# Performance work log

Measured on AMD Instinct MI355X. Metric: run time of the kernel, lower is better.

Reference implementation:

```python
import jax, jax.numpy as jnp
import numpy as np

B, T, C, H = 2, 2048, 1024, 16
HD = C // H  # 64

def setup_inputs() -> dict:
    key = jax.random.key(0)
    ks = jax.random.split(key, 9)
    s = 0.02
    return {
        "x": jax.random.normal(ks[0], (B, T, C), jnp.float32),
        "Wq": jax.random.normal(ks[1], (C, C), jnp.float32) * s,
        "bq": jax.random.normal(ks[2], (C,), jnp.float32) * s,
        "Wk": jax.random.normal(ks[3], (C, C), jnp.float32) * s,
        "bk": jax.random.normal(ks[4], (C,), jnp.float32) * s,
        "Wv": jax.random.normal(ks[5], (C, C), jnp.float32) * s,
        "bv": jax.random.normal(ks[6], (C,), jnp.float32) * s,
        "Wp": jax.random.normal(ks[7], (C, C), jnp.float32) * s,
        "bp": jax.random.normal(ks[8], (C,), jnp.float32) * s,
    }

def reference(x, Wq, bq, Wk, bk, Wv, bv, Wp, bp):
    Bb, Tt, Cc = x.shape
    hd = Cc // H
    # project and split heads: [B, H, T, hd]
    def heads(W, b):
        return (x @ W.T + b).reshape(Bb, Tt, H, hd).transpose(0, 2, 1, 3)
    q, k, v = heads(Wq, bq), heads(Wk, bk), heads(Wv, bv)
    scale = 1.0 / np.sqrt(hd).astype(np.float32)
    att = jnp.einsum('bhqd,bhkd->bhqk', q, k) * scale
    causal = jnp.tril(jnp.ones((Tt, Tt), bool))
    att = jnp.where(causal[None, None], att, -jnp.inf)
    att = jax.nn.softmax(att, axis=-1)
    y = jnp.einsum('bhqk,bhkd->bhqd', att, v)
    y = y.transpose(0, 2, 1, 3).reshape(Bb, Tt, Cc)
    return y @ Wp.T + bp
```

## Files before the change

kernel.cpp:

```cpp
#include <hip/hip_runtime.h>
#include <hip/hip_bf16.h>

#define Tsz 2048
#define Csz 1024
#define Hn 16

typedef short s8v __attribute__((ext_vector_type(8)));
typedef short s4v __attribute__((ext_vector_type(4)));
typedef float f4v __attribute__((ext_vector_type(4)));
typedef int   i4v __attribute__((ext_vector_type(4)));
typedef unsigned u2v __attribute__((ext_vector_type(2)));

#define QSCALE (0.125f * 1.44269504088896f)

__device__ __forceinline__ unsigned short bfr(float x) {
    return (unsigned short)((__builtin_bit_cast(unsigned, x) + 0x8000u) >> 16);
}
__device__ __forceinline__ unsigned pack2_rn(float a, float b) {
    const unsigned ua = __builtin_bit_cast(unsigned, a) + 0x8000u;
    const unsigned ub = __builtin_bit_cast(unsigned, b) + 0x8000u;
    return (ua >> 16) | (ub & 0xFFFF0000u);
}

__device__ __forceinline__ void gload_lds(const void* g, void* l) {
    __builtin_amdgcn_global_load_lds(
        (const __attribute__((address_space(1))) void*)g,
        (__attribute__((address_space(3))) void*)l, 16, 0, 0);
}

__global__ void cvt6(const float* __restrict__ x, const float* __restrict__ wq,
                     const float* __restrict__ wk, const float* __restrict__ wv,
                     const float* __restrict__ wp,
                     short* __restrict__ xo, short* __restrict__ qo,
                     short* __restrict__ ko, short* __restrict__ vo,
                     short* __restrict__ po) {
    const int bx = blockIdx.x;
    const float* in; short* out; int ib;
    if (bx < 4096) { in = x; out = xo; ib = bx; }
    else {
        const int r = bx - 4096, w = r >> 10;
        ib = r & 1023;
        switch (w) {
            case 0: in = wq; out = qo; break;
            case 1: in = wk; out = ko; break;
            case 2: in = wv; out = vo; break;
            default: in = wp; out = po; break;
        }
    }
    const int i = ib * 1024 + threadIdx.x * 4;
    float4 v = *(const float4*)(in + i);
    int2 o;
    o.x = (int)pack2_rn(v.x, v.y);
    o.y = (int)pack2_rn(v.z, v.w);
    *(int2*)(out + i) = o;
}

__global__ __launch_bounds__(256, 3) void qkv_gemm(
    const short* __restrict__ X,
    const short* __restrict__ Wq, const short* __restrict__ Wk, const short* __restrict__ Wv,
    const float* __restrict__ bq, const float* __restrict__ bk, const float* __restrict__ bv,
    short* __restrict__ Qo, short* __restrict__ Ko, short* __restrict__ Vto)
{
    const int z = blockIdx.z;
    const short* W = (z == 0) ? Wq : (z == 1) ? Wk : Wv;
    const float* bias = (z == 0) ? bq : (z == 1) ? bk : bv;

    __shared__ __align__(16) short Ash[128 * 32];
    __shared__ __align__(16) short Bsh[128 * 32];
    __shared__ __align__(16) short TR[64 * 72];

    const int tid = threadIdx.x, lane = tid & 63, wave = tid >> 6;
    const int ln = lane & 15, hi = lane >> 4;
    const int m0 = blockIdx.x * 128, n0 = blockIdx.y * 128;
    const int wm = (wave >> 1) * 64, wn = (wave & 1) * 64;

    const short* Ag = X + (size_t)(m0 + (tid >> 2)) * Csz + (tid & 3) * 8;
    const short* Bg = W + (size_t)(n0 + (tid >> 2)) * Csz + (tid & 3) * 8;

    f4v acc[4][4];
    #pragma unroll
    for (int mt = 0; mt < 4; mt++)
        #pragma unroll
        for (int nt = 0; nt < 4; nt++)
            #pragma unroll
            for (int i = 0; i < 4; i++) acc[mt][nt][i] = 0.f;

    for (int k0 = 0; k0 < Csz; k0 += 32) {
        __syncthreads();
        gload_lds(Ag + k0, Ash + tid * 8);
        gload_lds(Ag + k0 + (size_t)64 * Csz, Ash + 2048 + tid * 8);
        gload_lds(Bg + k0, Bsh + tid * 8);
        gload_lds(Bg + k0 + (size_t)64 * Csz, Bsh + 2048 + tid * 8);
        __syncthreads();

        s8v af[4], bfr_[4];
        #pragma unroll
        for (int mt = 0; mt < 4; mt++)
            af[mt] = *(const s8v*)(Ash + (wm + mt * 16 + ln) * 32 + hi * 8);
        #pragma unroll
        for (int nt = 0; nt < 4; nt++)
            bfr_[nt] = *(const s8v*)(Bsh + (wn + nt * 16 + ln) * 32 + hi * 8);
        #pragma unroll
        for (int mt = 0; mt < 4; mt++)
            #pragma unroll
            for (int nt = 0; nt < 4; nt++)
                acc[mt][nt] = __builtin_amdgcn_mfma_f32_16x16x32_bf16(af[mt], bfr_[nt], acc[mt][nt], 0, 0, 0);
    }

    if (z == 2) {
        const int b = m0 >> 11, t0 = m0 & 2047;
        float bvv[4];
        #pragma unroll
        for (int nt = 0; nt < 4; nt++) bvv[nt] = bias[n0 + wn + nt * 16 + ln];
        #pragma unroll
        for (int ph = 0; ph < 4; ph++) {
            const int mh = ph >> 1, nh = ph & 1;
            __syncthreads();
            if ((wave >> 1) == mh && (wave & 1) == nh) {
                #pragma unroll
                for (int mt = 0; mt < 4; mt++)
                    #pragma unroll
                    for (int nt = 0; nt < 4; nt++) {
                        int2 pk;
                        pk.x = (int)pack2_rn(acc[mt][nt][0] + bvv[nt], acc[mt][nt][1] + bvv[nt]);
                        pk.y = (int)pack2_rn(acc[mt][nt][2] + bvv[nt], acc[mt][nt][3] + bvv[nt]);
                        *(int2*)(TR + (nt * 16 + ln) * 72 + mt * 16 + hi * 4) = pk;
                    }
            }
            __syncthreads();
            const int chl = tid >> 2, seg = tid & 3;
            const s8v r0 = *(const s8v*)(TR + chl * 72 + seg * 16);
            const s8v r1 = *(const s8v*)(TR + chl * 72 + seg * 16 + 8);
            short* dst = Vto + (size_t)(b * 1024 + n0 + nh * 64 + chl) * Tsz + t0 + mh * 64 + seg * 16;
            *(s8v*)(dst) = r0;
            *(s8v*)(dst + 8) = r1;
        }
        return;
    }

    const float scale = (z == 0) ? QSCALE : 1.0f;
    short* out = (z == 0) ? Qo : Ko;

    #pragma unroll
    for (int nt = 0; nt < 4; nt++) {
        const int col = n0 + wn + nt * 16 + ln;
        const float bvv = bias[col];
        #pragma unroll
        for (int mt = 0; mt < 4; mt++) {
            const int row0 = m0 + wm + mt * 16 + hi * 4;
            #pragma unroll
            for (int i = 0; i < 4; i++)
                out[(size_t)(row0 + i) * Csz + col] = (short)bfr((acc[mt][nt][i] + bvv) * scale);
        }
    }
}

__global__ __launch_bounds__(256, 2) void proj_gemm(
    const short* __restrict__ A, const short* __restrict__ W,
    const float* __restrict__ bias, float* __restrict__ out)
{
    __shared__ __align__(16) short Ash[128 * 32];
    __shared__ __align__(16) short Bsh[64 * 32];

    const int tid = threadIdx.x, lane = tid & 63, wave = tid >> 6;
    const int ln = lane & 15, hi = lane >> 4;
    const int m0 = blockIdx.x * 128, n0 = blockIdx.y * 64;
    const int wm = (wave >> 1) * 64, wn = (wave & 1) * 32;

    const short* Ag = A + (size_t)(m0 + (tid >> 2)) * Csz + (tid & 3) * 8;
    const short* Bg = W + (size_t)(n0 + (tid >> 2)) * Csz + (tid & 3) * 8;

    f4v acc[4][2];
    #pragma unroll
    for (int mt = 0; mt < 4; mt++)
        #pragma unroll
        for (int nt = 0; nt < 2; nt++)
            #pragma unroll
            for (int i = 0; i < 4; i++) acc[mt][nt][i] = 0.f;

    for (int k0 = 0; k0 < Csz; k0 += 32) {
        __syncthreads();
        gload_lds(Ag + k0, Ash + tid * 8);
        gload_lds(Ag + k0 + (size_t)64 * Csz, Ash + 2048 + tid * 8);
        gload_lds(Bg + k0, Bsh + tid * 8);
        __syncthreads();

        s8v af[4], bfr_[2];
        #pragma unroll
        for (int mt = 0; mt < 4; mt++)
            af[mt] = *(const s8v*)(Ash + (wm + mt * 16 + ln) * 32 + hi * 8);
        #pragma unroll
        for (int nt = 0; nt < 2; nt++)
            bfr_[nt] = *(const s8v*)(Bsh + (wn + nt * 16 + ln) * 32 + hi * 8);
        #pragma unroll
        for (int mt = 0; mt < 4; mt++)
            #pragma unroll
            for (int nt = 0; nt < 2; nt++)
                acc[mt][nt] = __builtin_amdgcn_mfma_f32_16x16x32_bf16(af[mt], bfr_[nt], acc[mt][nt], 0, 0, 0);
    }

    #pragma unroll
    for (int nt = 0; nt < 2; nt++) {
        const int col = n0 + wn + nt * 16 + ln;
        const float bvv = bias[col];
        #pragma unroll
        for (int mt = 0; mt < 4; mt++)
            #pragma unroll
            for (int i = 0; i < 4; i++)
                out[(size_t)(m0 + wm + mt * 16 + hi * 4 + i) * Csz + col] = acc[mt][nt][i] + bvv;
    }
}

__global__ __launch_bounds__(256, 4) void attn14(
    const short* __restrict__ Q, const short* __restrict__ Kg,
    const short* __restrict__ Vt, short* __restrict__ Y)
{
    __shared__ __align__(16) short Ksh[64 * 64];
    __shared__ __align__(16) short Vsh[64 * 64];

    const int tid = threadIdx.x, lane = tid & 63, wave = tid >> 6;
    const int ln = lane & 15, hi = lane >> 4;

    const int n = blockIdx.x;
    const int c = n & 255, j = n >> 8;
    const int bh = (j << 3) | (c >> 5);
    const int t = c & 31;
    const int qt = (j & 1) ? t : 31 - t;

    const size_t base = (size_t)(bh >> 4) * Tsz * Csz + (size_t)(bh & 15) * 64;
    const size_t vtbase = (size_t)bh * 64 * Tsz;
    const int qrel = wave * 16 + ln;

    s8v qf[2];
    #pragma unroll
    for (int kk = 0; kk < 2; kk++)
        qf[kk] = *(const s8v*)(Q + base + (size_t)(qt * 64 + qrel) * Csz + kk * 32 + hi * 8);

    f4v o[4];
    float lsum = 0.f;
    #pragma unroll
    for (int dt = 0; dt < 4; dt++)
        #pragma unroll
        for (int i = 0; i < 4; i++) o[dt][i] = 0.f;

    const int sr = tid >> 3, scs = tid & 7;
    const short* Kp = Kg + base + (size_t)sr * Csz + scs * 8;
    const short* Vp = Vt + vtbase + (size_t)sr * Tsz + scs * 8;
    const int swo = sr * 64 + (scs ^ (sr & 7)) * 8;
    const int nkb = qt + 1;

    int foff[2][4];
    #pragma unroll
    for (int nt = 0; nt < 4; nt++)
        #pragma unroll
        for (int kk = 0; kk < 2; kk++)
            foff[kk][nt] = (nt * 16 + ln) * 64 + (((kk * 4 + hi) ^ (ln & 7)) * 8);

    s8v k0 = *(const s8v*)(Kp);
    s8v k1 = *(const s8v*)(Kp + (size_t)32 * Csz);
    s8v v0 = *(const s8v*)(Vp);
    s8v v1 = *(const s8v*)(Vp + (size_t)32 * Tsz);
    *(s8v*)(&Ksh[swo]) = k0;
    *(s8v*)(&Ksh[swo + 32 * 64]) = k1;
    *(s8v*)(&Vsh[swo]) = v0;
    *(s8v*)(&Vsh[swo + 32 * 64]) = v1;
    __syncthreads();

    for (int kb = 0; kb < nkb; kb++) {
        const bool more = (kb + 1 < nkb);
        if (more) {
            const size_t ko = (size_t)(kb + 1) * 64;
            k0 = *(const s8v*)(Kp + ko * Csz);
            k1 = *(const s8v*)(Kp + (ko + 32) * Csz);
            v0 = *(const s8v*)(Vp + ko);
            v1 = *(const s8v*)(Vp + ko + (size_t)32 * Tsz);
        }

        s8v kf[2][4], vf[2][4];
        #pragma unroll
        for (int nt = 0; nt < 4; nt++)
            #pragma unroll
            for (int kk = 0; kk < 2; kk++) {
                kf[kk][nt] = *(const s8v*)(&Ksh[foff[kk][nt]]);
                vf[kk][nt] = *(const s8v*)(&Vsh[foff[kk][nt]]);
            }

        f4v s[4];
        #pragma unroll
        for (int nt = 0; nt < 4; nt++) {
            #pragma unroll
            for (int i = 0; i < 4; i++) s[nt][i] = 0.f;
            s[nt] = __builtin_amdgcn_mfma_f32_16x16x32_bf16(kf[0][nt], qf[0], s[nt], 0, 0, 0);
            s[nt] = __builtin_amdgcn_mfma_f32_16x16x32_bf16(kf[1][nt], qf[1], s[nt], 0, 0, 0);
        }

        const bool dg = !more;
        unsigned pw[4][2];
        #pragma unroll
        for (int nt = 0; nt < 4; nt++) {
            float pv[4];
            #pragma unroll
            for (int i = 0; i < 4; i++) pv[i] = exp2f(s[nt][i]);
            if (dg) {
                const int kr = nt * 16 + hi * 4;
                #pragma unroll
                for (int i = 0; i < 4; i++)
                    if (kr + i > qrel) pv[i] = 0.f;
            }
            lsum += (pv[0] + pv[1]) + (pv[2] + pv[3]);
            pw[nt][0] = pack2_rn(pv[0], pv[1]);
            pw[nt][1] = pack2_rn(pv[2], pv[3]);
        }

        u2v r0a = __builtin_amdgcn_permlane32_swap(pw[0][0], pw[1][0], false, false);
        u2v r0b = __builtin_amdgcn_permlane16_swap(r0a[0], r0a[1], false, false);
        u2v r1a = __builtin_amdgcn_permlane32_swap(pw[0][1], pw[1][1], false, false);
        u2v r1b = __builtin_amdgcn_permlane16_swap(r1a[0], r1a[1], false, false);
        u2v r2a = __builtin_amdgcn_permlane32_swap(pw[2][0], pw[3][0], false, false);
        u2v r2b = __builtin_amdgcn_permlane16_swap(r2a[0], r2a[1], false, false);
        u2v r3a = __builtin_amdgcn_permlane32_swap(pw[2][1], pw[3][1], false, false);
        u2v r3b = __builtin_amdgcn_permlane16_swap(r3a[0], r3a[1], false, false);
        i4v p0 = { (int)r0b[0], (int)r1b[0], (int)r0b[1], (int)r1b[1] };
        i4v p1 = { (int)r2b[0], (int)r3b[0], (int)r2b[1], (int)r3b[1] };
        const s8v pb0 = __builtin_bit_cast(s8v, p0);
        const s8v pb1 = __builtin_bit_cast(s8v, p1);

        #pragma unroll
        for (int dt = 0; dt < 4; dt++) {
            o[dt] = __builtin_amdgcn_mfma_f32_16x16x32_bf16(vf[0][dt], pb0, o[dt], 0, 0, 0);
            o[dt] = __builtin_amdgcn_mfma_f32_16x16x32_bf16(vf[1][dt], pb1, o[dt], 0, 0, 0);
        }

        if (more) {
            __syncthreads();
            *(s8v*)(&Ksh[swo]) = k0;
            *(s8v*)(&Ksh[swo + 32 * 64]) = k1;
            *(s8v*)(&Vsh[swo]) = v0;
            *(s8v*)(&Vsh[swo + 32 * 64]) = v1;
            __syncthreads();
        }
    }

    float l = lsum;
    l += __shfl_xor(l, 16);
    l += __shfl_xor(l, 32);
    const float inv = 1.0f / l;
    const int qrow = qt * 64 + qrel;
    #pragma unroll
    for (int dt = 0; dt < 4; dt++) {
        int2 w;
        w.x = (int)pack2_rn(o[dt][0] * inv, o[dt][1] * inv);
        w.y = (int)pack2_rn(o[dt][2] * inv, o[dt][3] * inv);
        *(int2*)(Y + base + (size_t)qrow * Csz + dt * 16 + hi * 4) = w;
    }
}

extern "C" void kernel_launch(void* const* d_in, const int* in_sizes, int n_in,
                              void* d_out, int out_size, void* d_ws, size_t ws_size,
                              hipStream_t stream) {
    const float* x  = (const float*)d_in[0];
    const float* Wq = (const float*)d_in[1];
    const float* bq = (const float*)d_in[2];
    const float* Wk = (const float*)d_in[3];
    const float* bk = (const float*)d_in[4];
    const float* Wv = (const float*)d_in[5];
    const float* bv = (const float*)d_in[6];
    const float* Wp = (const float*)d_in[7];
    const float* bp = (const float*)d_in[8];

    char* ws = (char*)d_ws;
    short* Xb  = (short*)(ws);
    short* Wqb = (short*)(ws + (8u  << 20));
    short* Wkb = (short*)(ws + (10u << 20));
    short* Wvb = (short*)(ws + (12u << 20));
    short* Wpb = (short*)(ws + (14u << 20));
    short* Qb  = (short*)(ws + (16u << 20));
    short* Kb  = (short*)(ws + (24u << 20));
    short* Vtb = (short*)(ws + (32u << 20));
    short* Yb  = (short*)(ws + (40u << 20));

    hipLaunchKernelGGL(cvt6, dim3(8192), dim3(256), 0, stream,
                       x, Wq, Wk, Wv, Wp, Xb, Wqb, Wkb, Wvb, Wpb);

    hipLaunchKernelGGL(qkv_gemm, dim3(32, 8, 3), dim3(256), 0, stream,
                       Xb, Wqb, Wkb, Wvb, bq, bk, bv, Qb, Kb, Vtb);

    hipLaunchKernelGGL(attn14, dim3(1024), dim3(256), 0, stream, Qb, Kb, Vtb, Yb);

    hipLaunchKernelGGL(proj_gemm, dim3(32, 16), dim3(256), 0, stream, Yb, Wpb, bp, (float*)d_out);
}
```

Before: 189.0 us.

## Triple-buffer K/V tiles in attention with direct global-to-LDS async loads

The attention kernel now stages K and V tiles straight from global memory into LDS with gload_lds into a three-slot ring buffer, prefetching two blocks ahead. It waits on vmcnt and uses a single barrier per iteration, replacing the register round-trip and the two __syncthreads per step. The swizzle moves from the LDS write offset to the global source column. Triple buffering raises LDS use to 48KB per block, so launch bounds drop from 4 to 3 blocks per CU, trading occupancy for deeper overlap of loads with compute.

Result: no change. 186.5 us (-1.3%).

```diff
diff --git a/kernel.cpp b/kernel.cpp
--- a/kernel.cpp
+++ b/kernel.cpp
@@ -211,12 +211,11 @@
     }
 }
 
-__global__ __launch_bounds__(256, 4) void attn14(
+__global__ __launch_bounds__(256, 3) void attn15(
     const short* __restrict__ Q, const short* __restrict__ Kg,
     const short* __restrict__ Vt, short* __restrict__ Y)
 {
-    __shared__ __align__(16) short Ksh[64 * 64];
-    __shared__ __align__(16) short Vsh[64 * 64];
+    __shared__ __align__(16) short SB[3][2][64 * 64];
 
     const int tid = threadIdx.x, lane = tid & 63, wave = tid >> 6;
     const int ln = lane & 15, hi = lane >> 4;
@@ -244,9 +243,11 @@
         for (int i = 0; i < 4; i++) o[dt][i] = 0.f;
 
     const int sr = tid >> 3, scs = tid & 7;
-    const short* Kp = Kg + base + (size_t)sr * Csz + scs * 8;
-    const short* Vp = Vt + vtbase + (size_t)sr * Tsz + scs * 8;
-    const int swo = sr * 64 + (scs ^ (sr & 7)) * 8;
+    const int csw = (scs ^ (sr & 7)) * 8;
+    const short* KpA = Kg + base + (size_t)sr * Csz + csw;
+    const short* KpB = KpA + (size_t)32 * Csz;
+    const short* VpA = Vt + vtbase + (size_t)sr * Tsz + csw;
+    const short* VpB = VpA + (size_t)32 * Tsz;
     const int nkb = qt + 1;
 
     int foff[2][4];
@@ -256,33 +257,36 @@
         for (int kk = 0; kk < 2; kk++)
             foff[kk][nt] = (nt * 16 + ln) * 64 + (((kk * 4 + hi) ^ (ln & 7)) * 8);
 
-    s8v k0 = *(const s8v*)(Kp);
-    s8v k1 = *(const s8v*)(Kp + (size_t)32 * Csz);
-    s8v v0 = *(const s8v*)(Vp);
-    s8v v1 = *(const s8v*)(Vp + (size_t)32 * Tsz);
-    *(s8v*)(&Ksh[swo]) = k0;
-    *(s8v*)(&Ksh[swo + 32 * 64]) = k1;
-    *(s8v*)(&Vsh[swo]) = v0;
-    *(s8v*)(&Vsh[swo + 32 * 64]) = v1;
-    __syncthreads();
-
+    #define STAGE(b, kb_) {                                              \
+        const size_t ko_ = (size_t)(kb_) * 64;                           \
+        gload_lds(KpA + ko_ * Csz, &SB[b][0][tid * 8]);                  \
+        gload_lds(KpB + ko_ * Csz, &SB[b][0][2048 + tid * 8]);           \
+        gload_lds(VpA + ko_,       &SB[b][1][tid * 8]);                  \
+        gload_lds(VpB + ko_,       &SB[b][1][2048 + tid * 8]);           \
+    }
+
+    STAGE(0, 0);
+    if (nkb > 1) {
+        STAGE(1, 1);
+        asm volatile("s_waitcnt vmcnt(4)" ::: "memory");
+    } else {
+        asm volatile("s_waitcnt vmcnt(0)" ::: "memory");
+    }
+    __builtin_amdgcn_s_barrier();
+
+    int bcur = 0, bnext = 1, bnn = 2;
     for (int kb = 0; kb < nkb; kb++) {
-        const bool more = (kb + 1 < nkb);
-        if (more) {
-            const size_t ko = (size_t)(kb + 1) * 64;
-            k0 = *(const s8v*)(Kp + ko * Csz);
-            k1 = *(const s8v*)(Kp + (ko + 32) * Csz);
-            v0 = *(const s8v*)(Vp + ko);
-            v1 = *(const s8v*)(Vp + ko + (size_t)32 * Tsz);
-        }
-
+        if (kb + 2 < nkb) STAGE(bnn, kb + 2);
+
+        const short* Kl = SB[bcur][0];
+        const short* Vl = SB[bcur][1];
         s8v kf[2][4], vf[2][4];
         #pragma unroll
         for (int nt = 0; nt < 4; nt++)
             #pragma unroll
             for (int kk = 0; kk < 2; kk++) {
-                kf[kk][nt] = *(const s8v*)(&Ksh[foff[kk][nt]]);
-                vf[kk][nt] = *(const s8v*)(&Vsh[foff[kk][nt]]);
+                kf[kk][nt] = *(const s8v*)(&Kl[foff[kk][nt]]);
+                vf[kk][nt] = *(const s8v*)(&Vl[foff[kk][nt]]);
             }
 
         f4v s[4];
@@ -294,7 +298,7 @@
             s[nt] = __builtin_amdgcn_mfma_f32_16x16x32_bf16(kf[1][nt], qf[1], s[nt], 0, 0, 0);
         }
 
-        const bool dg = !more;
+        const bool dg = (kb == qt);
         unsigned pw[4][2];
         #pragma unroll
         for (int nt = 0; nt < 4; nt++) {
@@ -331,15 +335,14 @@
             o[dt] = __builtin_amdgcn_mfma_f32_16x16x32_bf16(vf[1][dt], pb1, o[dt], 0, 0, 0);
         }
 
-        if (more) {
-            __syncthreads();
-            *(s8v*)(&Ksh[swo]) = k0;
-            *(s8v*)(&Ksh[swo + 32 * 64]) = k1;
-            *(s8v*)(&Vsh[swo]) = v0;
-            *(s8v*)(&Vsh[swo + 32 * 64]) = v1;
-            __syncthreads();
-        }
-    }
+        if (kb + 1 < nkb) {
+            if (kb + 2 < nkb) asm volatile("s_waitcnt vmcnt(4)" ::: "memory");
+            else              asm volatile("s_waitcnt vmcnt(0)" ::: "memory");
+            __builtin_amdgcn_s_barrier();
+        }
+        const int tb = bcur; bcur = bnext; bnext = bnn; bnn = tb;
+    }
+    #undef STAGE
 
     float l = lsum;
     l += __shfl_xor(l, 16);
@@ -385,7 +388,7 @@
     hipLaunchKernelGGL(qkv_gemm, dim3(32, 8, 3), dim3(256), 0, stream,
                        Xb, Wqb, Wkb, Wvb, bq, bk, bv, Qb, Kb, Vtb);
 
-    hipLaunchKernelGGL(attn14, dim3(1024), dim3(256), 0, stream, Qb, Kb, Vtb, Yb);
+    hipLaunchKernelGGL(attn15, dim3(1024), dim3(256), 0, stream, Qb, Kb, Vtb, Yb);
 
     hipLaunchKernelGGL(proj_gemm, dim3(32, 16), dim3(256), 0, stream, Yb, Wpb, bp, (float*)d_out);
 }
```
